# Performance work log

Hardware: AMD Instinct MI355X
Metric: run time of the kernel (lower is better)

## Reference

```python
import jax, jax.numpy as jnp
import numpy as np
import math

B, S, D, H = 4, 2048, 1024, 16
DK = D // H

def setup_inputs() -> dict:
    key = jax.random.key(0)
    ks = jax.random.split(key, 6)
    scale = 1.0 / math.sqrt(D)
    x = jax.random.normal(ks[0], (B, S, D), dtype=jnp.float32)
    mask = jnp.tril(jnp.ones((S, S), dtype=jnp.int32))[None, None]  # [1,1,S,S] causal
    Wq = jax.random.normal(ks[1], (D, D), dtype=jnp.float32) * scale
    Wk = jax.random.normal(ks[2], (D, D), dtype=jnp.float32) * scale
    Wv = jax.random.normal(ks[3], (D, D), dtype=jnp.float32) * scale
    Wo = jax.random.normal(ks[4], (D, D), dtype=jnp.float32) * scale
    z = jnp.zeros((D,), dtype=jnp.float32)
    return {"x": x, "mask": mask, "Wq": Wq, "bq": z, "Wk": Wk, "bk": z,
            "Wv": Wv, "bv": z, "Wo": Wo, "bo": z}

def reference(x, mask, Wq, bq, Wk, bk, Wv, bv, Wo, bo):
    bsz, seq_len, d_model = x.shape
    def split_heads(t):  # [B,S,D] -> [B,H,S,DK]
        return t.reshape(bsz, seq_len, H, DK).transpose(0, 2, 1, 3)
    Q = split_heads(x @ Wq + bq)
    K = split_heads(x @ Wk + bk)
    V = split_heads(x @ Wv + bv)
    scores = jnp.einsum('bhqd,bhkd->bhqk', Q, K) / jnp.sqrt(jnp.asarray(DK, x.dtype))
    scores = jnp.where(mask == 0, jnp.asarray(-jnp.inf, x.dtype), scores)
    attn = jax.nn.softmax(scores, axis=-1)
    # dropout is identity in eval mode
    context = jnp.einsum('bhqk,bhkd->bhqd', attn, V)
    context = context.transpose(0, 2, 1, 3).reshape(bsz, seq_len, d_model)
    return context @ Wo + bo
```

## Files before the change

### kernel.cpp

```cpp
#include <hip/hip_runtime.h>
#include <hip/hip_bf16.h>
#include <math.h>

#define BATCH 4
#define SEQ   2048
#define DMODEL 1024
#define NHEAD 16
#define DHEAD 64
#define MROWS (BATCH * SEQ)
#define SC_Q  0.1803368801111244f

typedef __attribute__((ext_vector_type(8))) short short8;
typedef __attribute__((ext_vector_type(4))) float f32x4;
typedef __attribute__((ext_vector_type(4))) unsigned short ushort4v;

__device__ inline unsigned short f2bf(float f) {
    union { float f; unsigned int u; } v; v.f = f;
    unsigned int r = v.u + 0x7FFFu + ((v.u >> 16) & 1u);
    return (unsigned short)(r >> 16);
}

__device__ inline unsigned int cvt_pk_bf16(float a, float b) {
    unsigned int r;
    asm("v_cvt_pk_bf16_f32 %0, %1, %2" : "=v"(r) : "v"(a), "v"(b));
    return r;
}

__device__ __forceinline__ void g2l16(const unsigned short* g, unsigned short* l) {
    __builtin_amdgcn_global_load_lds(
        (const __attribute__((address_space(1))) unsigned int*)g,
        (__attribute__((address_space(3))) unsigned int*)l, 16, 0, 0);
}

__global__ __launch_bounds__(256) void cvt_bf16_kernel(
    const float* __restrict__ src, unsigned short* __restrict__ dst, int n4)
{
    const int i = blockIdx.x * 256 + threadIdx.x;
    if (i < n4) {
        float4 v = ((const float4*)src)[i];
        ushort4v o = { f2bf(v.x), f2bf(v.y), f2bf(v.z), f2bf(v.w) };
        ((ushort4v*)dst)[i] = o;
    }
}

__global__ __launch_bounds__(256) void bias_pack_kernel(
    const float* __restrict__ bq, const float* __restrict__ bk,
    const float* __restrict__ bv, float* __restrict__ b3)
{
    const int i = blockIdx.x * 256 + threadIdx.x;
    if (i < DMODEL) {
        b3[i]              = bq[i];
        b3[i + DMODEL]     = bk[i];
        b3[i + 2 * DMODEL] = bv[i];
    }
}

__global__ __launch_bounds__(256) void transpose_cvt_kernel(
    const float* __restrict__ W0, const float* __restrict__ W1,
    const float* __restrict__ W2, const float* __restrict__ W3,
    unsigned short* __restrict__ T0, unsigned short* __restrict__ T1,
    unsigned short* __restrict__ T2, unsigned short* __restrict__ T3)
{
    const float* W; unsigned short* T;
    switch (blockIdx.z) {
        case 0: W = W0; T = T0; break;
        case 1: W = W1; T = T1; break;
        case 2: W = W2; T = T2; break;
        default: W = W3; T = T3; break;
    }
    __shared__ float tile[32][33];
    const int r0 = blockIdx.y * 32, c0 = blockIdx.x * 32;
    const int c = threadIdx.x & 31, r = threadIdx.x >> 5;
    #pragma unroll
    for (int i = 0; i < 4; ++i)
        tile[r + i * 8][c] = W[(size_t)(r0 + r + i * 8) * DMODEL + c0 + c];
    __syncthreads();
    #pragma unroll
    for (int i = 0; i < 4; ++i)
        T[(size_t)(c0 + r + i * 8) * DMODEL + r0 + c] = f2bf(tile[c][r + i * 8]);
}

__global__ __launch_bounds__(256) void transpose_v_kernel(
    const unsigned short* __restrict__ Vin, unsigned short* __restrict__ Vt)
{
    __shared__ unsigned short t[64][72];
    const int tid = threadIdx.x;
    const int kt = blockIdx.x, bh = blockIdx.y;
    const unsigned short* src = Vin + ((size_t)bh * SEQ + kt * 64) * DHEAD;
    const int r = tid >> 3, c = (tid & 7) * 8;
    *(short8*)&t[r][c]      = *(const short8*)(src + (size_t)r * DHEAD + c);
    *(short8*)&t[r + 32][c] = *(const short8*)(src + (size_t)(r + 32) * DHEAD + c);
    __syncthreads();
    unsigned short* dst = Vt + (size_t)bh * DHEAD * SEQ + kt * 64;
    const int d = tid >> 3, p0 = (tid & 7) * 8;
    short8 v0, v1;
    #pragma unroll
    for (int i = 0; i < 8; ++i) {
        const int p = p0 + i;
        const int k = (p & 32) | (((p >> 2) & 1) << 4) | (((p >> 3) & 3) << 2) | (p & 3);
        v0[i] = (short)t[k][d];
        v1[i] = (short)t[k][d + 32];
    }
    *(short8*)(dst + (size_t)d * SEQ + p0)        = v0;
    *(short8*)(dst + (size_t)(d + 32) * SEQ + p0) = v1;
}

__device__ __forceinline__ void gemm_main_256x128(
    const unsigned short* __restrict__ A, const unsigned short* __restrict__ Bt,
    f32x4 (&acc)[4][4], int m0, int n0, int wm, int wn, int l15, int quad)
{
    __shared__ unsigned short As[2][256 * 64];
    __shared__ unsigned short Bs[2][128 * 64];

    const int tid = threadIdx.x;

    #pragma unroll
    for (int i = 0; i < 4; ++i)
        #pragma unroll
        for (int j = 0; j < 4; ++j) acc[i][j] = (f32x4){0.f, 0.f, 0.f, 0.f};

    const unsigned short* gA[4];
    const unsigned short* gB[2];
    #pragma unroll
    for (int j = 0; j < 4; ++j) {
        const int c = tid + j * 512, row = c >> 3, gq = (c & 7) ^ (row & 7);
        gA[j] = A + (size_t)(m0 + row) * DMODEL + gq * 8;
    }
    #pragma unroll
    for (int j = 0; j < 2; ++j) {
        const int c = tid + j * 512, row = c >> 3, gq = (c & 7) ^ (row & 7);
        gB[j] = Bt + (size_t)(n0 + row) * DMODEL + gq * 8;
    }

    #define STAGE2(buf)                                                        \
        do {                                                                   \
            _Pragma("unroll")                                                  \
            for (int j = 0; j < 4; ++j) {                                      \
                g2l16(gA[j], &As[buf][(tid + j * 512) * 8]); gA[j] += 64;      \
            }                                                                  \
            _Pragma("unroll")                                                  \
            for (int j = 0; j < 2; ++j) {                                      \
                g2l16(gB[j], &Bs[buf][(tid + j * 512) * 8]); gB[j] += 64;      \
            }                                                                  \
        } while (0)

    STAGE2(0);

    const int NT = DMODEL / 64;
    #pragma unroll 2
    for (int t = 0; t < NT; ++t) {
        const int cur = t & 1;
        if (t + 1 < NT) {
            STAGE2(cur ^ 1);
            asm volatile("s_waitcnt vmcnt(6)" ::: "memory");
        } else {
            asm volatile("s_waitcnt vmcnt(0)" ::: "memory");
        }
        __syncthreads();

        short8 bfr[4][2];
        #pragma unroll
        for (int ni = 0; ni < 4; ++ni) {
            const int row = wn + ni * 16 + l15;
            const unsigned short* bp = &Bs[cur][row * 64];
            bfr[ni][0] = *(const short8*)(bp + ((    quad) ^ (row & 7)) * 8);
            bfr[ni][1] = *(const short8*)(bp + ((4 + quad) ^ (row & 7)) * 8);
        }
        #pragma unroll
        for (int pp = 0; pp < 2; ++pp) {
            short8 af[2][2];
            #pragma unroll
            for (int mm = 0; mm < 2; ++mm) {
                const int row = wm + (pp * 2 + mm) * 16 + l15;
                const unsigned short* ap = &As[cur][row * 64];
                af[mm][0] = *(const short8*)(ap + ((    quad) ^ (row & 7)) * 8);
                af[mm][1] = *(const short8*)(ap + ((4 + quad) ^ (row & 7)) * 8);
            }
            __builtin_amdgcn_s_setprio(1);
            #pragma unroll
            for (int mm = 0; mm < 2; ++mm)
                #pragma unroll
                for (int ni = 0; ni < 4; ++ni) {
                    acc[pp * 2 + mm][ni] = __builtin_amdgcn_mfma_f32_16x16x32_bf16(
                        af[mm][0], bfr[ni][0], acc[pp * 2 + mm][ni], 0, 0, 0);
                    acc[pp * 2 + mm][ni] = __builtin_amdgcn_mfma_f32_16x16x32_bf16(
                        af[mm][1], bfr[ni][1], acc[pp * 2 + mm][ni], 0, 0, 0);
                }
            __builtin_amdgcn_s_setprio(0);
        }
        __syncthreads();
    }
    #undef STAGE2
}

__global__ __launch_bounds__(512, 2) void gemm_qkv(
    const unsigned short* __restrict__ A, const unsigned short* __restrict__ Bt,
    const float* __restrict__ bias3, unsigned short* __restrict__ QKV )
{
    const int tid  = threadIdx.x;
    const int wave = tid >> 6, lane = tid & 63;
    const int l15  = lane & 15, quad = lane >> 4;
    const int wm   = (wave >> 1) * 64;
    const int wn   = (wave & 1) * 64;
    const int m0   = blockIdx.y * 256;
    const int n0   = blockIdx.x * 128;

    f32x4 acc[4][4];
    gemm_main_256x128(A, Bt, acc, m0, n0, wm, wn, l15, quad);

    const size_t elems = (size_t)MROWS * DMODEL;
    #pragma unroll
    for (int mi = 0; mi < 4; ++mi) {
        #pragma unroll
        for (int r = 0; r < 4; ++r) {
            const int m = m0 + wm + mi * 16 + quad * 4 + r;
            const int b = m >> 11, s = m & 2047;
            #pragma unroll
            for (int ni = 0; ni < 4; ++ni) {
                const int n   = n0 + wn + ni * 16 + l15;
                const int seg = n >> 10, nn = n & 1023;
                const int h = nn >> 6, dk = nn & 63;
                const float sc  = (seg == 0) ? SC_Q : 1.0f;
                const float val = (acc[mi][ni][r] + bias3[n]) * sc;
                QKV[seg * elems + (((size_t)(b * NHEAD + h)) * SEQ + s) * DHEAD + dk] = f2bf(val);
            }
        }
    }
}

__global__ __launch_bounds__(512, 2) void gemm_out(
    const unsigned short* __restrict__ A, const unsigned short* __restrict__ Bt,
    const float* __restrict__ bias, float* __restrict__ Cout)
{
    const int tid  = threadIdx.x;
    const int wave = tid >> 6, lane = tid & 63;
    const int l15  = lane & 15, quad = lane >> 4;
    const int wm   = (wave >> 1) * 64;
    const int wn   = (wave & 1) * 64;
    const int m0   = blockIdx.y * 256;
    const int n0   = blockIdx.x * 128;

    f32x4 acc[4][4];
    gemm_main_256x128(A, Bt, acc, m0, n0, wm, wn, l15, quad);

    #pragma unroll
    for (int mi = 0; mi < 4; ++mi) {
        #pragma unroll
        for (int r = 0; r < 4; ++r) {
            const int m = m0 + wm + mi * 16 + quad * 4 + r;
            #pragma unroll
            for (int ni = 0; ni < 4; ++ni) {
                const int n = n0 + wn + ni * 16 + l15;
                Cout[(size_t)m * DMODEL + n] = acc[mi][ni][r] + bias[n];
            }
        }
    }
}

__global__ __launch_bounds__(256, 4) void attn_mfma7(
    const unsigned short* __restrict__ Q, const unsigned short* __restrict__ K,
    const unsigned short* __restrict__ VtG, unsigned short* __restrict__ ctx_out)
{
    __shared__ alignas(16) unsigned short Ks[2][64 * 64];
    __shared__ alignas(16) unsigned short Vs[2][64 * 64];

    const int tid  = threadIdx.x;
    const int wave = tid >> 6, lane = tid & 63;
    const int l15  = lane & 15, quad = lane >> 4;
    const int qa   = blockIdx.x;
    const int qb   = 31 - qa;
    const int bh   = blockIdx.y;
    const int b    = bh >> 4, h = bh & 15;

    const unsigned short* Kb0 = K   + (size_t)bh * SEQ * DHEAD;
    const unsigned short* Vb0 = VtG + (size_t)bh * DHEAD * SEQ;

    short8 qf[2][2];
    #pragma unroll
    for (int g = 0; g < 2; ++g) {
        const int qtile = g ? qb : qa;
        const unsigned short* qrow =
            Q + ((size_t)bh * SEQ + qtile * 64 + wave * 16 + l15) * DHEAD + quad * 8;
        qf[g][0] = *(const short8*)qrow;
        qf[g][1] = *(const short8*)(qrow + 32);
    }

    f32x4 Of[2][4];
    float lsum[2] = {0.f, 0.f};
    #pragma unroll
    for (int g = 0; g < 2; ++g)
        #pragma unroll
        for (int i = 0; i < 4; ++i) Of[g][i] = (f32x4){0.f, 0.f, 0.f, 0.f};

    const int qloc = wave * 16 + l15;
    const f32x4 zero4 = (f32x4){0.f, 0.f, 0.f, 0.f};

    const int ck0 = tid >> 3, cg0 = tid & 7;
    const int ck1 = (tid + 256) >> 3, cg1 = tid & 7;

    #define STAGE(buf, jb)                                                          \
        do {                                                                        \
            const unsigned short* Kt_ = Kb0 + (size_t)(jb) * 64 * DHEAD;            \
            const unsigned short* Vt_ = Vb0 + (jb) * 64;                            \
            g2l16(Kt_ + (size_t)ck0 * DHEAD + (cg0 ^ (ck0 & 7)) * 8,                \
                  &Ks[buf][(tid) * 8]);                                             \
            g2l16(Vt_ + (size_t)ck0 * SEQ   + (cg0 ^ (ck0 & 7)) * 8,                \
                  &Vs[buf][(tid) * 8]);                                             \
            g2l16(Kt_ + (size_t)ck1 * DHEAD + (cg1 ^ (ck1 & 7)) * 8,                \
                  &Ks[buf][(tid + 256) * 8]);                                       \
            g2l16(Vt_ + (size_t)ck1 * SEQ   + (cg1 ^ (ck1 & 7)) * 8,                \
                  &Vs[buf][(tid + 256) * 8]);                                       \
        } while (0)

    STAGE(0, 0);

    for (int jb = 0; jb <= qb; ++jb) {
        const int cur = jb & 1;
        asm volatile("s_waitcnt vmcnt(0)" ::: "memory");
        __syncthreads();
        if (jb < qb) STAGE(cur ^ 1, jb + 1);

        const bool act0  = (jb <= qa);
        const bool diag0 = (jb == qa);
        const bool diag1 = (jb == qb);
        const unsigned short* KsC = &Ks[cur][0];
        const unsigned short* VsC = &Vs[cur][0];

        union { unsigned int u[4]; short8 v; } pa[2][2];
        #pragma unroll
        for (int nt = 0; nt < 4; ++nt) {
            const int k = nt * 16 + l15;
            const short8 a0 = *(const short8*)&KsC[(k * 8 + ( quad      ^ (k & 7))) * 8];
            const short8 a1 = *(const short8*)&KsC[(k * 8 + ((quad + 4) ^ (k & 7))) * 8];

            f32x4 s1 = __builtin_amdgcn_mfma_f32_16x16x32_bf16(a0, qf[1][0], zero4, 0, 0, 0);
            s1       = __builtin_amdgcn_mfma_f32_16x16x32_bf16(a1, qf[1][1], s1,    0, 0, 0);
            f32x4 p1;
            #pragma unroll
            for (int r = 0; r < 4; ++r) p1[r] = __builtin_amdgcn_exp2f(s1[r]);
            if (diag1) {
                #pragma unroll
                for (int r = 0; r < 4; ++r)
                    if (nt * 16 + quad * 4 + r > qloc) p1[r] = 0.f;
            }
            lsum[1] += (p1[0] + p1[1]) + (p1[2] + p1[3]);
            pa[1][nt >> 1].u[(nt & 1) * 2]     = cvt_pk_bf16(p1[0], p1[1]);
            pa[1][nt >> 1].u[(nt & 1) * 2 + 1] = cvt_pk_bf16(p1[2], p1[3]);

            if (act0) {
                f32x4 s0 = __builtin_amdgcn_mfma_f32_16x16x32_bf16(a0, qf[0][0], zero4, 0, 0, 0);
                s0       = __builtin_amdgcn_mfma_f32_16x16x32_bf16(a1, qf[0][1], s0,    0, 0, 0);
                f32x4 p0;
                #pragma unroll
                for (int r = 0; r < 4; ++r) p0[r] = __builtin_amdgcn_exp2f(s0[r]);
                if (diag0) {
                    #pragma unroll
                    for (int r = 0; r < 4; ++r)
                        if (nt * 16 + quad * 4 + r > qloc) p0[r] = 0.f;
                }
                lsum[0] += (p0[0] + p0[1]) + (p0[2] + p0[3]);
                pa[0][nt >> 1].u[(nt & 1) * 2]     = cvt_pk_bf16(p0[0], p0[1]);
                pa[0][nt >> 1].u[(nt & 1) * 2 + 1] = cvt_pk_bf16(p0[2], p0[3]);
            }
        }

        #pragma unroll
        for (int cc = 0; cc < 2; ++cc) {
            #pragma unroll
            for (int nt = 0; nt < 4; ++nt) {
                const int d = nt * 16 + l15;
                const short8 vb = *(const short8*)
                    &VsC[(d * 8 + ((cc * 4 + quad) ^ (d & 7))) * 8];
                Of[1][nt] = __builtin_amdgcn_mfma_f32_16x16x32_bf16(
                    pa[1][cc].v, vb, Of[1][nt], 0, 0, 0);
                if (act0)
                    Of[0][nt] = __builtin_amdgcn_mfma_f32_16x16x32_bf16(
                        pa[0][cc].v, vb, Of[0][nt], 0, 0, 0);
            }
        }
    }
    #undef STAGE

    #pragma unroll
    for (int g = 0; g < 2; ++g) {
        const int qtile = g ? qb : qa;
        float l = lsum[g];
        l += __shfl_xor(l, 16);
        l += __shfl_xor(l, 32);
        #pragma unroll
        for (int r = 0; r < 4; ++r) {
            const float inv = 1.0f / __shfl(l, quad * 4 + r);
            const int s = qtile * 64 + wave * 16 + quad * 4 + r;
            unsigned short* o = ctx_out + ((size_t)(b * SEQ + s)) * DMODEL + h * DHEAD;
            #pragma unroll
            for (int nt = 0; nt < 4; ++nt)
                o[nt * 16 + l15] = f2bf(Of[g][nt][r] * inv);
        }
    }
}

extern "C" void kernel_launch(void* const* d_in, const int* in_sizes, int n_in,
                              void* d_out, int out_size, void* d_ws, size_t ws_size,
                              hipStream_t stream) {
    const float* x  = (const float*)d_in[0];
    const float* Wq = (const float*)d_in[2];
    const float* bq = (const float*)d_in[3];
    const float* Wk = (const float*)d_in[4];
    const float* bk = (const float*)d_in[5];
    const float* Wv = (const float*)d_in[6];
    const float* bv = (const float*)d_in[7];
    const float* Wo = (const float*)d_in[8];
    const float* bo = (const float*)d_in[9];
    float* out = (float*)d_out;

    const size_t elems  = (size_t)MROWS * DMODEL;
    const size_t welems = (size_t)DMODEL * DMODEL;
    unsigned short* xbf   = (unsigned short*)d_ws;
    unsigned short* WqkvT = xbf + elems;
    unsigned short* WoT   = WqkvT + 3 * welems;
    unsigned short* Qbuf  = WoT + welems;
    unsigned short* Kbuf  = Qbuf + elems;
    unsigned short* Vbuf  = Kbuf + elems;
    unsigned short* VtG   = Vbuf + elems;
    unsigned short* Cbuf  = VtG + elems;
    float*          bias3 = (float*)(Cbuf + elems);

    dim3 blk(256);
    dim3 blk2(512);

    cvt_bf16_kernel<<<dim3((int)(elems / 4 / 256)), blk, 0, stream>>>(x, xbf, (int)(elems / 4));
    transpose_cvt_kernel<<<dim3(32, 32, 4), blk, 0, stream>>>(
        Wq, Wk, Wv, Wo, WqkvT, WqkvT + welems, WqkvT + 2 * welems, WoT);
    bias_pack_kernel<<<dim3(4), blk, 0, stream>>>(bq, bk, bv, bias3);

    dim3 gqkv(3 * DMODEL / 128, MROWS / 256);
    gemm_qkv<<<gqkv, blk2, 0, stream>>>(xbf, WqkvT, bias3, Qbuf);

    transpose_v_kernel<<<dim3(SEQ / 64, BATCH * NHEAD), blk, 0, stream>>>(Vbuf, VtG);

    dim3 gattn(16, BATCH * NHEAD);
    attn_mfma7<<<gattn, blk, 0, stream>>>(Qbuf, Kbuf, VtG, Cbuf);

    dim3 gout(DMODEL / 128, MROWS / 256);
    gemm_out<<<gout, blk2, 0, stream>>>(Cbuf, WoT, bo, out);
}
```

Before: 295.7 us.

## Restructure GEMM mainloop into triple-buffered 8-phase barrier-interleaved pipeline

Replaces the double-buffered GEMM mainloop with a triple-buffered scheme. Each K-tile is split into four phases of LDS reads and MFMAs, with global-to-LDS loads for the tile two steps ahead interleaved between them and s_barrier calls separating the phases. The aim is to hide load latency and overlap memory with MFMA work more finely. The cost is 50% more LDS, which may drop occupancy to one block per CU, plus many more barriers.

```diff
diff --git a/kernel.cpp b/kernel.cpp
--- a/kernel.cpp
+++ b/kernel.cpp
@@ -31,6 +31,8 @@
         (const __attribute__((address_space(1))) unsigned int*)g,
         (__attribute__((address_space(3))) unsigned int*)l, 16, 0, 0);
 }
+
+#define SBAR()  do { __builtin_amdgcn_s_barrier(); asm volatile("" ::: "memory"); } while (0)
 
 __global__ __launch_bounds__(256) void cvt_bf16_kernel(
     const float* __restrict__ src, unsigned short* __restrict__ dst, int n4)
@@ -105,12 +107,12 @@
     *(short8*)(dst + (size_t)(d + 32) * SEQ + p0) = v1;
 }
 
-__device__ __forceinline__ void gemm_main_256x128(
+__device__ __forceinline__ void gemm_main_8ph(
     const unsigned short* __restrict__ A, const unsigned short* __restrict__ Bt,
     f32x4 (&acc)[4][4], int m0, int n0, int wm, int wn, int l15, int quad)
 {
-    __shared__ unsigned short As[2][256 * 64];
-    __shared__ unsigned short Bs[2][128 * 64];
+    __shared__ unsigned short As[3][256 * 64];
+    __shared__ unsigned short Bs[3][128 * 64];
 
     const int tid = threadIdx.x;
 
@@ -121,76 +123,114 @@
 
     const unsigned short* gA[4];
     const unsigned short* gB[2];
+    int cA[4], cB[2];
     #pragma unroll
     for (int j = 0; j < 4; ++j) {
         const int c = tid + j * 512, row = c >> 3, gq = (c & 7) ^ (row & 7);
         gA[j] = A + (size_t)(m0 + row) * DMODEL + gq * 8;
+        cA[j] = c * 8;
     }
     #pragma unroll
     for (int j = 0; j < 2; ++j) {
         const int c = tid + j * 512, row = c >> 3, gq = (c & 7) ^ (row & 7);
         gB[j] = Bt + (size_t)(n0 + row) * DMODEL + gq * 8;
-    }
-
-    #define STAGE2(buf)                                                        \
-        do {                                                                   \
-            _Pragma("unroll")                                                  \
-            for (int j = 0; j < 4; ++j) {                                      \
-                g2l16(gA[j], &As[buf][(tid + j * 512) * 8]); gA[j] += 64;      \
-            }                                                                  \
-            _Pragma("unroll")                                                  \
-            for (int j = 0; j < 2; ++j) {                                      \
-                g2l16(gB[j], &Bs[buf][(tid + j * 512) * 8]); gB[j] += 64;      \
-            }                                                                  \
-        } while (0)
-
-    STAGE2(0);
-
-    const int NT = DMODEL / 64;
-    #pragma unroll 2
-    for (int t = 0; t < NT; ++t) {
-        const int cur = t & 1;
-        if (t + 1 < NT) {
-            STAGE2(cur ^ 1);
+        cB[j] = c * 8;
+    }
+
+    #pragma unroll
+    for (int tt = 0; tt < 2; ++tt) {
+        #pragma unroll
+        for (int j = 0; j < 4; ++j) { g2l16(gA[j], &As[tt][cA[j]]); gA[j] += 64; }
+        #pragma unroll
+        for (int j = 0; j < 2; ++j) { g2l16(gB[j], &Bs[tt][cB[j]]); gB[j] += 64; }
+    }
+    asm volatile("s_waitcnt vmcnt(6)" ::: "memory");
+    SBAR();
+
+    int cur = 0, sb = 2;
+    #pragma unroll 1
+    for (int t = 0; t < DMODEL / 64; ++t) {
+        const unsigned short* As_c = &As[cur][0];
+        const unsigned short* Bs_c = &Bs[cur][0];
+        unsigned short* As_s = &As[sb][0];
+        unsigned short* Bs_s = &Bs[sb][0];
+        const bool st = (t < DMODEL / 64 - 2);
+
+        const int rm0 = wm + l15,      rm1 = wm + 16 + l15;
+        const int rm2 = wm + 32 + l15, rm3 = wm + 48 + l15;
+        short8 bfr[4], a0, a1;
+
+        #pragma unroll
+        for (int ni = 0; ni < 4; ++ni) {
+            const int rn = wn + ni * 16 + l15;
+            bfr[ni] = *(const short8*)&Bs_c[rn * 64 + (quad ^ (rn & 7)) * 8];
+        }
+        a0 = *(const short8*)&As_c[rm0 * 64 + (quad ^ (rm0 & 7)) * 8];
+        a1 = *(const short8*)&As_c[rm1 * 64 + (quad ^ (rm1 & 7)) * 8];
+        if (st) { g2l16(gA[0], &As_s[cA[0]]); gA[0] += 64;
+                  g2l16(gA[1], &As_s[cA[1]]); gA[1] += 64; }
+        SBAR();
+        __builtin_amdgcn_s_setprio(1);
+        #pragma unroll
+        for (int ni = 0; ni < 4; ++ni) {
+            acc[0][ni] = __builtin_amdgcn_mfma_f32_16x16x32_bf16(a0, bfr[ni], acc[0][ni], 0, 0, 0);
+            acc[1][ni] = __builtin_amdgcn_mfma_f32_16x16x32_bf16(a1, bfr[ni], acc[1][ni], 0, 0, 0);
+        }
+        __builtin_amdgcn_s_setprio(0);
+        SBAR();
+
+        a0 = *(const short8*)&As_c[rm2 * 64 + (quad ^ (rm2 & 7)) * 8];
+        a1 = *(const short8*)&As_c[rm3 * 64 + (quad ^ (rm3 & 7)) * 8];
+        if (st) { g2l16(gA[2], &As_s[cA[2]]); gA[2] += 64;
+                  g2l16(gA[3], &As_s[cA[3]]); gA[3] += 64; }
+        SBAR();
+        __builtin_amdgcn_s_setprio(1);
+        #pragma unroll
+        for (int ni = 0; ni < 4; ++ni) {
+            acc[2][ni] = __builtin_amdgcn_mfma_f32_16x16x32_bf16(a0, bfr[ni], acc[2][ni], 0, 0, 0);
+            acc[3][ni] = __builtin_amdgcn_mfma_f32_16x16x32_bf16(a1, bfr[ni], acc[3][ni], 0, 0, 0);
+        }
+        __builtin_amdgcn_s_setprio(0);
+        SBAR();
+
+        #pragma unroll
+        for (int ni = 0; ni < 4; ++ni) {
+            const int rn = wn + ni * 16 + l15;
+            bfr[ni] = *(const short8*)&Bs_c[rn * 64 + ((4 + quad) ^ (rn & 7)) * 8];
+        }
+        a0 = *(const short8*)&As_c[rm0 * 64 + ((4 + quad) ^ (rm0 & 7)) * 8];
+        a1 = *(const short8*)&As_c[rm1 * 64 + ((4 + quad) ^ (rm1 & 7)) * 8];
+        if (st) { g2l16(gB[0], &Bs_s[cB[0]]); gB[0] += 64;
+                  g2l16(gB[1], &Bs_s[cB[1]]); gB[1] += 64; }
+        SBAR();
+        __builtin_amdgcn_s_setprio(1);
+        #pragma unroll
+        for (int ni = 0; ni < 4; ++ni) {
+            acc[0][ni] = __builtin_amdgcn_mfma_f32_16x16x32_bf16(a0, bfr[ni], acc[0][ni], 0, 0, 0);
+            acc[1][ni] = __builtin_amdgcn_mfma_f32_16x16x32_bf16(a1, bfr[ni], acc[1][ni], 0, 0, 0);
+        }
+        __builtin_amdgcn_s_setprio(0);
+        SBAR();
+
+        a0 = *(const short8*)&As_c[rm2 * 64 + ((4 + quad) ^ (rm2 & 7)) * 8];
+        a1 = *(const short8*)&As_c[rm3 * 64 + ((4 + quad) ^ (rm3 & 7)) * 8];
+        if (st)
             asm volatile("s_waitcnt vmcnt(6)" ::: "memory");
-        } else {
+        else if (t == DMODEL / 64 - 2)
             asm volatile("s_waitcnt vmcnt(0)" ::: "memory");
-        }
-        __syncthreads();
-
-        short8 bfr[4][2];
-        #pragma unroll
-        for (int ni = 0; ni < 4; ++ni) {
-            const int row = wn + ni * 16 + l15;
-            const unsigned short* bp = &Bs[cur][row * 64];
-            bfr[ni][0] = *(const short8*)(bp + ((    quad) ^ (row & 7)) * 8);
-            bfr[ni][1] = *(const short8*)(bp + ((4 + quad) ^ (row & 7)) * 8);
-        }
-        #pragma unroll
-        for (int pp = 0; pp < 2; ++pp) {
-            short8 af[2][2];
-            #pragma unroll
-            for (int mm = 0; mm < 2; ++mm) {
-                const int row = wm + (pp * 2 + mm) * 16 + l15;
-                const unsigned short* ap = &As[cur][row * 64];
-                af[mm][0] = *(const short8*)(ap + ((    quad) ^ (row & 7)) * 8);
-                af[mm][1] = *(const short8*)(ap + ((4 + quad) ^ (row & 7)) * 8);
-            }
-            __builtin_amdgcn_s_setprio(1);
-            #pragma unroll
-            for (int mm = 0; mm < 2; ++mm)
-                #pragma unroll
-                for (int ni = 0; ni < 4; ++ni) {
-                    acc[pp * 2 + mm][ni] = __builtin_amdgcn_mfma_f32_16x16x32_bf16(
-                        af[mm][0], bfr[ni][0], acc[pp * 2 + mm][ni], 0, 0, 0);
-                    acc[pp * 2 + mm][ni] = __builtin_amdgcn_mfma_f32_16x16x32_bf16(
-                        af[mm][1], bfr[ni][1], acc[pp * 2 + mm][ni], 0, 0, 0);
-                }
-            __builtin_amdgcn_s_setprio(0);
-        }
-        __syncthreads();
-    }
-    #undef STAGE2
+        SBAR();
+        __builtin_amdgcn_s_setprio(1);
+        #pragma unroll
+        for (int ni = 0; ni < 4; ++ni) {
+            acc[2][ni] = __builtin_amdgcn_mfma_f32_16x16x32_bf16(a0, bfr[ni], acc[2][ni], 0, 0, 0);
+            acc[3][ni] = __builtin_amdgcn_mfma_f32_16x16x32_bf16(a1, bfr[ni], acc[3][ni], 0, 0, 0);
+        }
+        __builtin_amdgcn_s_setprio(0);
+        SBAR();
+
+        cur = (cur == 2) ? 0 : cur + 1;
+        sb  = (sb  == 2) ? 0 : sb  + 1;
+    }
 }
 
 __global__ __launch_bounds__(512, 2) void gemm_qkv(
@@ -206,7 +246,7 @@
     const int n0   = blockIdx.x * 128;
 
     f32x4 acc[4][4];
-    gemm_main_256x128(A, Bt, acc, m0, n0, wm, wn, l15, quad);
+    gemm_main_8ph(A, Bt, acc, m0, n0, wm, wn, l15, quad);
 
     const size_t elems = (size_t)MROWS * DMODEL;
     #pragma unroll
@@ -241,7 +281,7 @@
     const int n0   = blockIdx.x * 128;
 
     f32x4 acc[4][4];
-    gemm_main_256x128(A, Bt, acc, m0, n0, wm, wn, l15, quad);
+    gemm_main_8ph(A, Bt, acc, m0, n0, wm, wn, l15, quad);
 
     #pragma unroll
     for (int mi = 0; mi < 4; ++mi) {
```

Result: faster. 283.9 us (-4.0%).
